# Kernel tuning notes

Measured on AMD Instinct MI355X. Metric: run time of the kernel, lower is better.

## Reference

```python
import jax, jax.numpy as jnp
import numpy as np

N_NODES = 50000
N_EDGES = 800000
N_HOPS = 4  # layers + 1
NFEAT, NHID, NOUT = 256, 128, 64


def setup_inputs() -> dict:
    key = jax.random.key(0)
    ks = jax.random.split(key, 8)
    x = jax.random.normal(ks[0], (N_NODES, NFEAT), dtype=jnp.float32)
    W = jax.random.normal(ks[1], (N_HOPS, NFEAT, NHID), dtype=jnp.float32) * 0.05
    b = jax.random.normal(ks[2], (N_HOPS, NHID), dtype=jnp.float32) * 0.05
    W_out = jax.random.normal(ks[3], (NHID * N_HOPS, NOUT), dtype=jnp.float32) * 0.05
    b_out = jax.random.normal(ks[4], (NOUT,), dtype=jnp.float32) * 0.05
    edge_rows = jax.random.randint(ks[5], (N_HOPS, N_EDGES), 0, N_NODES, dtype=jnp.int32)
    edge_cols = jax.random.randint(ks[6], (N_HOPS, N_EDGES), 0, N_NODES, dtype=jnp.int32)
    edge_vals = jax.random.uniform(ks[7], (N_HOPS, N_EDGES), dtype=jnp.float32)
    return {"x": x, "W": W, "b": b, "W_out": W_out, "b_out": b_out,
            "edge_rows": edge_rows, "edge_cols": edge_cols, "edge_vals": edge_vals}


def reference(x, W, b, W_out, b_out, edge_rows, edge_cols, edge_vals):
    # per-hop linear: [N, nfeat] x [K, nfeat, nhid] -> [K, N, nhid]
    h = jnp.einsum('nf,kfh->knh', x, W) + b[:, None, :]

    def spmm(rows, cols, vals, feat):
        # COO spmm: out[r] += vals[e] * feat[cols[e]]
        return jax.ops.segment_sum(vals[:, None] * feat[cols], rows,
                                   num_segments=N_NODES)

    agg = jax.vmap(spmm)(edge_rows, edge_cols, edge_vals, h)  # [K, N, nhid]
    # concat across hops along feature dim (matches torch.cat order)
    concat = jnp.transpose(agg, (1, 0, 2)).reshape(x.shape[0], -1)  # [N, K*nhid]
    z = jax.nn.elu(concat)
    return z @ W_out + b_out  # [N, nout]
```

## Files before the change

### kernel.cpp

```cpp
#include <hip/hip_runtime.h>
#include <hip/hip_bf16.h>
#include <math.h>

#define NNODES 50000
#define NPAD   50176
#define NEDGES 800000
#define NHOPS  4
#define NF     256
#define NH     128
#define NO     64
#define NB     196
#define EPB    4096

#define CONVX_BLOCKS 12500
#define CONVW_BLOCKS 512
#define HIST1_BLOCKS (NB * NHOPS)
#define WOT_BLOCKS   128
#define LIN_PER_HOP  391
#define LIN_BLOCKS   1568
#define ASTR 40
#define CPAD 132

typedef __attribute__((ext_vector_type(8))) short bfrag_t;
typedef __attribute__((ext_vector_type(4))) float facc_t;

static __device__ __forceinline__ unsigned short f2bf(float f) {
  unsigned int u = __float_as_uint(f);
  unsigned int r = (u + 0x7fffu + ((u >> 16) & 1u)) >> 16;
  return (unsigned short)r;
}
static __device__ __forceinline__ float bf2f_lo(unsigned int u) {
  return __uint_as_float(u << 16);
}
static __device__ __forceinline__ float bf2f_hi(unsigned int u) {
  return __uint_as_float(u & 0xffff0000u);
}

__global__ __launch_bounds__(256) void phaseA_kernel(
    const float* __restrict__ x, unsigned short* __restrict__ xb,
    const float* __restrict__ W, unsigned short* __restrict__ Wt,
    const int* __restrict__ erows, int* __restrict__ bucketCur,
    const float* __restrict__ Wout, unsigned short* __restrict__ wot) {
  const int bx = blockIdx.x;
  const int t  = threadIdx.x;
  if (bx < CONVX_BLOCKS) {
    const size_t i = ((size_t)bx * 256 + t) * 4;
    float4 v = *(const float4*)&x[i];
    ushort4 o;
    o.x = f2bf(v.x); o.y = f2bf(v.y); o.z = f2bf(v.z); o.w = f2bf(v.w);
    *(ushort4*)&xb[i] = o;
  } else if (bx < CONVX_BLOCKS + CONVW_BLOCKS) {
    const int i = (bx - CONVX_BLOCKS) * 256 + t;
    const int k = i / (NH * NF);
    const int rem = i - k * NH * NF;
    const int n = rem / NF;
    const int f = rem - n * NF;
    Wt[i] = f2bf(W[(size_t)k * NF * NH + (size_t)f * NH + n]);
  } else if (bx < CONVX_BLOCKS + CONVW_BLOCKS + HIST1_BLOCKS) {
    const int id  = bx - (CONVX_BLOCKS + CONVW_BLOCKS);
    const int hop = id / NB;
    const int bb  = (id - hop * NB) * EPB;
    __shared__ int bh[NB];
    for (int i = t; i < NB; i += 256) bh[i] = 0;
    __syncthreads();
    const size_t g0 = (size_t)hop * NEDGES;
#pragma unroll
    for (int k = 0; k < 4; ++k) {
      const int e0 = bb + t * 4 + k * 1024;
      if (e0 + 3 < NEDGES) {
        const int4 rr = *(const int4*)&erows[g0 + e0];
        atomicAdd(&bh[rr.x >> 8], 1);
        atomicAdd(&bh[rr.y >> 8], 1);
        atomicAdd(&bh[rr.z >> 8], 1);
        atomicAdd(&bh[rr.w >> 8], 1);
      } else {
        for (int j = 0; j < 4; ++j)
          if (e0 + j < NEDGES) atomicAdd(&bh[erows[g0 + e0 + j] >> 8], 1);
      }
    }
    __syncthreads();
    for (int i = t; i < NB; i += 256)
      if (bh[i]) atomicAdd(&bucketCur[hop * NB + i], bh[i]);
  } else {
    const int i = (bx - (CONVX_BLOCKS + CONVW_BLOCKS + HIST1_BLOCKS)) * 256 + t;
    const int o = i & 63;
    const int f = i >> 6;
    wot[(size_t)o * 512 + f] = f2bf(Wout[(size_t)f * NO + o]);
  }
}

__global__ __launch_bounds__(256) void scanB_kernel(
    int* __restrict__ bucketCur, int* __restrict__ bucketBase) {
  const int hop = blockIdx.x;
  const int t   = threadIdx.x;
  __shared__ int tot[NB];
  for (int i = t; i < NB; i += 256) tot[i] = bucketCur[hop * NB + i];
  __syncthreads();
  if (t == 0) {
    int run = 0;
    for (int i = 0; i < NB; ++i) { const int c = tot[i]; tot[i] = run; run += c; }
  }
  __syncthreads();
  for (int i = t; i < NB; i += 256) {
    bucketCur[hop * NB + i]        = tot[i];
    bucketBase[hop * (NB + 1) + i] = tot[i];
  }
  if (t == 0) bucketBase[hop * (NB + 1) + NB] = NEDGES;
}

__global__ __launch_bounds__(256) void linear_kernel(
    const unsigned short* __restrict__ xb, const unsigned short* __restrict__ Wt,
    const float* __restrict__ b, unsigned short* __restrict__ slots) {
  const int lb  = blockIdx.x;
  const int g   = lb >> 5;
  const int rr_ = lb & 31;
  const int hop = rr_ >> 3;
  const int xx  = rr_ & 7;
  const int mb  = g * 8 + xx;
  if (mb >= LIN_PER_HOP) return;
  const unsigned short* Wk = Wt + (size_t)hop * NH * NF;
  const float* bk = b + hop * NH;
  unsigned short* hb = slots + (size_t)(hop + 1) * NNODES * NH;

  const int t    = threadIdx.x;
  const int lane = t & 63;
  const int wave = t >> 6;
  const int wm   = (wave >> 1) * 64;
  const int wn   = (wave & 1) * 64;
  const int m0   = mb * 128;
  const int l15  = lane & 15;
  const int quad = lane >> 4;

  __shared__ unsigned short smem[10240];
  unsigned short* as_ = smem;
  unsigned short* cs  = smem;

  facc_t acc[4][4];
#pragma unroll
  for (int i = 0; i < 4; ++i)
#pragma unroll
    for (int j = 0; j < 4; ++j) {
      facc_t z = {0.f, 0.f, 0.f, 0.f};
      acc[i][j] = z;
    }

#pragma unroll
  for (int k0 = 0; k0 < NF; k0 += 32) {
    __syncthreads();
#pragma unroll
    for (int it = 0; it < 2; ++it) {
      const int row = it * 64 + (t >> 2);
      const int ch  = t & 3;
      const uint4 v = *(const uint4*)&xb[(size_t)(m0 + row) * NF + k0 + ch * 8];
      *(uint4*)&as_[row * ASTR + ch * 8] = v;
    }
    __syncthreads();

    bfrag_t a[4], bb[4];
#pragma unroll
    for (int mi = 0; mi < 4; ++mi)
      a[mi] = *(const bfrag_t*)&as_[(wm + mi * 16 + l15) * ASTR + quad * 8];
#pragma unroll
    for (int ni = 0; ni < 4; ++ni) {
      const int n = wn + ni * 16 + l15;
      bb[ni] = *(const bfrag_t*)&Wk[(size_t)n * NF + k0 + quad * 8];
    }
#pragma unroll
    for (int mi = 0; mi < 4; ++mi)
#pragma unroll
      for (int ni = 0; ni < 4; ++ni)
        acc[mi][ni] = __builtin_amdgcn_mfma_f32_16x16x32_bf16(
            a[mi], bb[ni], acc[mi][ni], 0, 0, 0);
  }

#pragma unroll
  for (int half = 0; half < 2; ++half) {
    __syncthreads();
    if ((wave >> 1) == half) {
#pragma unroll
      for (int ni = 0; ni < 4; ++ni) {
        const int nl = wn + ni * 16 + l15;
        const float bias = bk[nl];
#pragma unroll
        for (int mi = 0; mi < 4; ++mi) {
#pragma unroll
          for (int r = 0; r < 4; ++r) {
            const int ml = mi * 16 + quad * 4 + r;
            cs[ml * CPAD + nl] = f2bf(acc[mi][ni][r] + bias);
          }
        }
      }
    }
    __syncthreads();
    const int chunk = t & 15;
    const int rowb  = t >> 4;
#pragma unroll
    for (int it = 0; it < 4; ++it) {
      const int row = it * 16 + rowb;
      const int m   = m0 + half * 64 + row;
      const uint4 v = *(const uint4*)&cs[row * CPAD + chunk * 8];
      if (m < NNODES) *(uint4*)&hb[(size_t)m * NH + chunk * 8] = v;
    }
  }
}

__global__ __launch_bounds__(256) void bin_kernel(
    const int* __restrict__ erows, const int* __restrict__ ecols,
    const float* __restrict__ evals, int* __restrict__ bucketCur,
    unsigned long long* __restrict__ staging) {
  const int hop = blockIdx.y;
  const int t   = threadIdx.x;
  const int bb  = blockIdx.x * EPB;
  __shared__ int lhist[NB];
  __shared__ int gbase[NB];
  for (int i = t; i < NB; i += 256) lhist[i] = 0;
  __syncthreads();

  unsigned long long pk[16];
  int bkt[16], rnk[16];
  const size_t g0 = (size_t)hop * NEDGES;
#pragma unroll
  for (int k = 0; k < 4; ++k) {
    const int e0 = bb + t * 4 + k * 1024;
    if (e0 + 3 < NEDGES) {
      const int4   rr = *(const int4*)&erows[g0 + e0];
      const int4   cc = *(const int4*)&ecols[g0 + e0];
      const float4 vv = *(const float4*)&evals[g0 + e0];
      const int r4[4] = {rr.x, rr.y, rr.z, rr.w};
      const int c4[4] = {cc.x, cc.y, cc.z, cc.w};
      const float v4[4] = {vv.x, vv.y, vv.z, vv.w};
#pragma unroll
      for (int j = 0; j < 4; ++j) {
        const int b = r4[j] >> 8;
        bkt[k * 4 + j] = b;
        rnk[k * 4 + j] = atomicAdd(&lhist[b], 1);
        pk[k * 4 + j] =
            ((unsigned long long)__float_as_uint(v4[j]) << 32) |
            ((unsigned)(r4[j] & 255) << 16) | (unsigned)c4[j];
      }
    } else {
#pragma unroll
      for (int j = 0; j < 4; ++j) {
        const int e = e0 + j;
        if (e < NEDGES) {
          const int r = erows[g0 + e];
          const int b = r >> 8;
          bkt[k * 4 + j] = b;
          rnk[k * 4 + j] = atomicAdd(&lhist[b], 1);
          pk[k * 4 + j] =
              ((unsigned long long)__float_as_uint(evals[g0 + e]) << 32) |
              ((unsigned)(r & 255) << 16) | (unsigned)ecols[g0 + e];
        } else {
          bkt[k * 4 + j] = -1;
        }
      }
    }
  }
  __syncthreads();
  for (int i = t; i < NB; i += 256) {
    const int c = lhist[i];
    gbase[i] = c ? atomicAdd(&bucketCur[hop * NB + i], c) : 0;
  }
  __syncthreads();
  unsigned long long* dst = staging + (size_t)hop * NEDGES;
#pragma unroll
  for (int q = 0; q < 16; ++q)
    if (bkt[q] >= 0) dst[gbase[bkt[q]] + rnk[q]] = pk[q];
}

__global__ __launch_bounds__(256) void countscan_kernel(
    const int* __restrict__ bucketBase,
    const unsigned long long* __restrict__ staging, int* __restrict__ counts) {
  const int hop = blockIdx.y;
  const int b   = blockIdx.x;
  const int t   = threadIdx.x;
  const int s = bucketBase[hop * (NB + 1) + b];
  const int e = bucketBase[hop * (NB + 1) + b + 1];
  __shared__ int h[256];
  h[t] = 0;
  __syncthreads();
  const unsigned long long* src = staging + (size_t)hop * NEDGES;
  for (int i = s + t; i < e; i += 256) {
    const int rl = ((unsigned)src[i] >> 16) & 255;
    atomicAdd(&h[rl], 1);
  }
  __syncthreads();
  const int r0 = b * 256;
  if (r0 + t < NNODES) counts[hop * NNODES + r0 + t] = h[t];
}

__global__ __launch_bounds__(1024) void scan_kernel(
    const int* __restrict__ counts, int* __restrict__ offs) {
  const int hop  = blockIdx.x;
  const int t    = threadIdx.x;
  const int lane = t & 63;
  const int wid  = t >> 6;
  __shared__ int wsum[16];
  __shared__ int carry_s;
  if (t == 0) carry_s = 0;
  __syncthreads();
  const int CH  = 8192;
  const int nch = (NNODES + CH - 1) / CH;
  for (int ch = 0; ch < nch; ++ch) {
    const int i0 = ch * CH + t * 8;
    int v[8];
    if (i0 + 7 < NNODES) {
      int4 a = *(const int4*)&counts[hop * NNODES + i0];
      int4 b = *(const int4*)&counts[hop * NNODES + i0 + 4];
      v[0]=a.x; v[1]=a.y; v[2]=a.z; v[3]=a.w;
      v[4]=b.x; v[5]=b.y; v[6]=b.z; v[7]=b.w;
    } else {
#pragma unroll
      for (int j = 0; j < 8; ++j)
        v[j] = (i0 + j < NNODES) ? counts[hop * NNODES + i0 + j] : 0;
    }
    int l[8];
    int run = 0;
#pragma unroll
    for (int j = 0; j < 8; ++j) { run += v[j]; l[j] = run; }
    int s = run;
#pragma unroll
    for (int d = 1; d < 64; d <<= 1) {
      int n = __shfl_up(s, d, 64);
      if (lane >= d) s += n;
    }
    if (lane == 63) wsum[wid] = s;
    __syncthreads();
    if (t < 16) {
      int ws = wsum[t];
#pragma unroll
      for (int d = 1; d < 16; d <<= 1) {
        int n = __shfl_up(ws, d, 16);
        if (t >= d) ws += n;
      }
      wsum[t] = ws;
    }
    __syncthreads();
    const int base = carry_s + (wid ? wsum[wid - 1] : 0) + (s - run);
    if (i0 + 7 < NNODES) {
      int4 o0 = make_int4(base, base + l[0], base + l[1], base + l[2]);
      int4 o1 = make_int4(base + l[3], base + l[4], base + l[5], base + l[6]);
      *(int4*)&offs[hop * (NNODES + 1) + i0]     = o0;
      *(int4*)&offs[hop * (NNODES + 1) + i0 + 4] = o1;
    } else {
#pragma unroll
      for (int j = 0; j < 8; ++j) {
        if (i0 + j < NNODES) {
          const int excl = base + (l[j] - v[j]);
          offs[hop * (NNODES + 1) + i0 + j] = excl;
        }
      }
    }
    __syncthreads();
    if (t == 0) carry_s += wsum[15];
    __syncthreads();
  }
  if (t == 0) offs[hop * (NNODES + 1) + NNODES] = carry_s;
}

__global__ __launch_bounds__(256) void place_kernel(
    const int* __restrict__ offs, const unsigned long long* __restrict__ staging,
    unsigned long long* __restrict__ ecsr) {
  const int hop = blockIdx.y;
  const int bk  = blockIdx.x;
  const int t   = threadIdx.x;
  const int r0  = bk * 256;
  const int nr  = (NNODES - r0 < 256) ? (NNODES - r0) : 256;
  const int* o = offs + (size_t)hop * (NNODES + 1);
  __shared__ int cur[257];
  for (int i = t; i <= nr; i += 256) cur[i] = o[r0 + i];
  __syncthreads();
  const int s = cur[0];
  const int e = cur[nr];
  __syncthreads();
  const unsigned long long* src = staging + (size_t)hop * NEDGES;
  unsigned long long* dst       = ecsr + (size_t)hop * NEDGES;
  for (int i = s + t; i < e; i += 256) {
    const unsigned long long v = src[i];
    const unsigned lo = (unsigned)v;
    const int rl = (lo >> 16) & 255;
    const int d = atomicAdd(&cur[rl], 1);
    dst[d] = (v & 0xFFFFFFFF00000000ull) | (unsigned long long)(lo & 0xFFFFu);
  }
}

__global__ __launch_bounds__(256) void gather_kernel(
    const int* __restrict__ offs, const int2* __restrict__ ecsr,
    const unsigned short* __restrict__ hb, unsigned short* __restrict__ aggb) {
  const int t    = threadIdx.x;
  const int lane = t & 63;
  const int wid  = t >> 6;
  const int r = blockIdx.x * 4 + wid;
  const int g  = lane >> 4;
  const int sl = lane & 15;
  const int s = offs[r];
  const int e = offs[r + 1];

  float acc[8];
#pragma unroll
  for (int j = 0; j < 8; ++j) acc[j] = 0.f;

  for (int p = s; p < e; p += 16) {
    int2 ed[4];
#pragma unroll
    for (int q = 0; q < 4; ++q) {
      const int idx = p + q * 4 + g;
      ed[q] = (idx < e) ? ecsr[idx] : make_int2(0, 0);
    }
    uint4 hv[4];
#pragma unroll
    for (int q = 0; q < 4; ++q)
      hv[q] = *(const uint4*)&hb[(size_t)ed[q].x * NH + sl * 8];
#pragma unroll
    for (int q = 0; q < 4; ++q) {
      const float v = __int_as_float(ed[q].y);
      acc[0] += v * bf2f_lo(hv[q].x);
      acc[1] += v * bf2f_hi(hv[q].x);
      acc[2] += v * bf2f_lo(hv[q].y);
      acc[3] += v * bf2f_hi(hv[q].y);
      acc[4] += v * bf2f_lo(hv[q].z);
      acc[5] += v * bf2f_hi(hv[q].z);
      acc[6] += v * bf2f_lo(hv[q].w);
      acc[7] += v * bf2f_hi(hv[q].w);
    }
  }

#pragma unroll
  for (int j = 0; j < 8; ++j) {
    acc[j] += __shfl_xor(acc[j], 16, 64);
    acc[j] += __shfl_xor(acc[j], 32, 64);
  }

  if (g == 0) {
    uint4 o;
    o.x = (unsigned)f2bf(acc[0]) | ((unsigned)f2bf(acc[1]) << 16);
    o.y = (unsigned)f2bf(acc[2]) | ((unsigned)f2bf(acc[3]) << 16);
    o.z = (unsigned)f2bf(acc[4]) | ((unsigned)f2bf(acc[5]) << 16);
    o.w = (unsigned)f2bf(acc[6]) | ((unsigned)f2bf(acc[7]) << 16);
    *(uint4*)&aggb[(size_t)r * NH + sl * 8] = o;
  }
}

__global__ __launch_bounds__(256) void out2_kernel(
    const unsigned short* __restrict__ aggb,
    const unsigned short* __restrict__ wot,
    const float* __restrict__ bout, float* __restrict__ out) {
  const int t    = threadIdx.x;
  const int lane = t & 63;
  const int wave = t >> 6;
  const int l15  = lane & 15;
  const int quad = lane >> 4;
  const int m0   = blockIdx.x * 64 + wave * 16;

  facc_t acc[4];
#pragma unroll
  for (int ni = 0; ni < 4; ++ni) { facc_t z = {0.f,0.f,0.f,0.f}; acc[ni] = z; }

  const int mrow  = m0 + l15;
  const int mload = mrow < NNODES ? mrow : NNODES - 1;

#pragma unroll
  for (int ks = 0; ks < 16; ++ks) {
    const int f0  = ks * 32 + quad * 8;
    const int hop = f0 >> 7;
    const int j0  = f0 & 127;
    uint4 ua = *(const uint4*)&aggb[((size_t)hop * NNODES + mload) * NH + j0];
    const unsigned uu[4] = {ua.x, ua.y, ua.z, ua.w};
    unsigned pr[4];
#pragma unroll
    for (int q = 0; q < 4; ++q) {
      float lo = bf2f_lo(uu[q]);
      float hi = bf2f_hi(uu[q]);
      lo = lo > 0.f ? lo : (expf(lo) - 1.f);
      hi = hi > 0.f ? hi : (expf(hi) - 1.f);
      pr[q] = (unsigned)f2bf(lo) | ((unsigned)f2bf(hi) << 16);
    }
    uint4 ra; ra.x = pr[0]; ra.y = pr[1]; ra.z = pr[2]; ra.w = pr[3];
    bfrag_t af = *(bfrag_t*)&ra;
    bfrag_t bf[4];
#pragma unroll
    for (int ni = 0; ni < 4; ++ni) {
      const int n = ni * 16 + l15;
      bf[ni] = *(const bfrag_t*)&wot[(size_t)n * 512 + f0];
    }
#pragma unroll
    for (int ni = 0; ni < 4; ++ni)
      acc[ni] = __builtin_amdgcn_mfma_f32_16x16x32_bf16(af, bf[ni], acc[ni], 0, 0, 0);
  }

#pragma unroll
  for (int ni = 0; ni < 4; ++ni) {
    const int o = ni * 16 + l15;
    const float bo = bout[o];
#pragma unroll
    for (int r = 0; r < 4; ++r) {
      const int m = m0 + quad * 4 + r;
      if (m < NNODES) out[(size_t)m * NO + o] = acc[ni][r] + bo;
    }
  }
}

extern "C" void kernel_launch(void* const* d_in, const int* in_sizes, int n_in,
                              void* d_out, int out_size, void* d_ws, size_t ws_size,
                              hipStream_t stream) {
  const float* x     = (const float*)d_in[0];
  const float* W     = (const float*)d_in[1];
  const float* b     = (const float*)d_in[2];
  const float* W_out = (const float*)d_in[3];
  const float* b_out = (const float*)d_in[4];
  const int*   erows = (const int*)d_in[5];
  const int*   ecols = (const int*)d_in[6];
  const float* evals = (const float*)d_in[7];
  float* out = (float*)d_out;

  unsigned short* slots = (unsigned short*)d_ws;
  unsigned short* xb = slots + (size_t)(NHOPS + 1) * NNODES * NH;
  unsigned short* Wt = xb + (size_t)NPAD * NF;
  unsigned long long* ecsr = (unsigned long long*)(Wt + (size_t)NHOPS * NH * NF);
  int* counts     = (int*)(ecsr + (size_t)NHOPS * NEDGES);
  int* offs       = counts + NHOPS * NNODES;
  int* bucketCur  = offs + NHOPS * (NNODES + 1);
  int* bucketBase = bucketCur + NHOPS * NB;
  unsigned short* wot = (unsigned short*)(bucketBase + NHOPS * (NB + 1));
  unsigned long long* staging = (unsigned long long*)xb;

  hipMemsetAsync(bucketCur, 0, (size_t)NHOPS * NB * sizeof(int), stream);

  phaseA_kernel<<<CONVX_BLOCKS + CONVW_BLOCKS + HIST1_BLOCKS + WOT_BLOCKS,
                  256, 0, stream>>>(x, xb, W, Wt, erows, bucketCur, W_out, wot);
  scanB_kernel<<<NHOPS, 256, 0, stream>>>(bucketCur, bucketBase);
  linear_kernel<<<LIN_BLOCKS, 256, 0, stream>>>(xb, Wt, b, slots);
  bin_kernel<<<dim3(NB, NHOPS), 256, 0, stream>>>(
      erows, ecols, evals, bucketCur, staging);
  countscan_kernel<<<dim3(NB, NHOPS), 256, 0, stream>>>(
      bucketBase, staging, counts);
  scan_kernel<<<NHOPS, 1024, 0, stream>>>(counts, offs);
  place_kernel<<<dim3(NB, NHOPS), 256, 0, stream>>>(offs, staging, ecsr);

  for (int k = 0; k < NHOPS; ++k) {
    gather_kernel<<<NNODES / 4, 256, 0, stream>>>(
        offs + (size_t)k * (NNODES + 1), (const int2*)(ecsr + (size_t)k * NEDGES),
        slots + (size_t)(k + 1) * NNODES * NH,
        slots + (size_t)k * NNODES * NH);
  }

  out2_kernel<<<782, 256, 0, stream>>>(slots, wot, b_out, out);
}
```

Measured before the change: 437.4 us.

## Batch hop gathers into paired launches and load GEMM A-fragments directly

Gathers for two hops now run in one 2D-grid launch. Outputs for hops 1 and 3 are redirected into the dead xb buffer so they do not overwrite inputs still being read, and out2 takes four separate aggregation pointers. The linear kernel drops LDS staging of the x tile and loads MFMA A-fragments straight from global memory, removing barriers but with less coalesced loads.

New measurement: 435.1 us. Within noise of the previous version (-0.5%).

```diff
diff --git a/kernel.cpp b/kernel.cpp
--- a/kernel.cpp
+++ b/kernel.cpp
@@ -18,7 +18,6 @@
 #define WOT_BLOCKS   128
 #define LIN_PER_HOP  391
 #define LIN_BLOCKS   1568
-#define ASTR 40
 #define CPAD 132
 
 typedef __attribute__((ext_vector_type(8))) short bfrag_t;
@@ -131,9 +130,7 @@
   const int l15  = lane & 15;
   const int quad = lane >> 4;
 
-  __shared__ unsigned short smem[10240];
-  unsigned short* as_ = smem;
-  unsigned short* cs  = smem;
+  __shared__ unsigned short cs[64 * CPAD];
 
   facc_t acc[4][4];
 #pragma unroll
@@ -146,20 +143,12 @@
 
 #pragma unroll
   for (int k0 = 0; k0 < NF; k0 += 32) {
-    __syncthreads();
-#pragma unroll
-    for (int it = 0; it < 2; ++it) {
-      const int row = it * 64 + (t >> 2);
-      const int ch  = t & 3;
-      const uint4 v = *(const uint4*)&xb[(size_t)(m0 + row) * NF + k0 + ch * 8];
-      *(uint4*)&as_[row * ASTR + ch * 8] = v;
-    }
-    __syncthreads();
-
     bfrag_t a[4], bb[4];
 #pragma unroll
-    for (int mi = 0; mi < 4; ++mi)
-      a[mi] = *(const bfrag_t*)&as_[(wm + mi * 16 + l15) * ASTR + quad * 8];
+    for (int mi = 0; mi < 4; ++mi) {
+      const int m = m0 + wm + mi * 16 + l15;
+      a[mi] = *(const bfrag_t*)&xb[(size_t)m * NF + k0 + quad * 8];
+    }
 #pragma unroll
     for (int ni = 0; ni < 4; ++ni) {
       const int n = wn + ni * 16 + l15;
@@ -384,17 +373,26 @@
   }
 }
 
-__global__ __launch_bounds__(256) void gather_kernel(
+__global__ __launch_bounds__(256) void gather2_kernel(
     const int* __restrict__ offs, const int2* __restrict__ ecsr,
-    const unsigned short* __restrict__ hb, unsigned short* __restrict__ aggb) {
+    const unsigned short* __restrict__ slots,
+    unsigned short* __restrict__ aggA, unsigned short* __restrict__ aggB,
+    int hop0) {
+  const int y    = blockIdx.y;
+  const int hop  = hop0 + y;
+  const int* off = offs + (size_t)hop * (NNODES + 1);
+  const int2* ec = ecsr + (size_t)hop * NEDGES;
+  const unsigned short* hb = slots + (size_t)(hop + 1) * NNODES * NH;
+  unsigned short* aggb = y ? aggB : aggA;
+
   const int t    = threadIdx.x;
   const int lane = t & 63;
   const int wid  = t >> 6;
   const int r = blockIdx.x * 4 + wid;
   const int g  = lane >> 4;
   const int sl = lane & 15;
-  const int s = offs[r];
-  const int e = offs[r + 1];
+  const int s = off[r];
+  const int e = off[r + 1];
 
   float acc[8];
 #pragma unroll
@@ -405,7 +403,7 @@
 #pragma unroll
     for (int q = 0; q < 4; ++q) {
       const int idx = p + q * 4 + g;
-      ed[q] = (idx < e) ? ecsr[idx] : make_int2(0, 0);
+      ed[q] = (idx < e) ? ec[idx] : make_int2(0, 0);
     }
     uint4 hv[4];
 #pragma unroll
@@ -442,7 +440,8 @@
 }
 
 __global__ __launch_bounds__(256) void out2_kernel(
-    const unsigned short* __restrict__ aggb,
+    const unsigned short* __restrict__ agg0, const unsigned short* __restrict__ agg1,
+    const unsigned short* __restrict__ agg2, const unsigned short* __restrict__ agg3,
     const unsigned short* __restrict__ wot,
     const float* __restrict__ bout, float* __restrict__ out) {
   const int t    = threadIdx.x;
@@ -464,7 +463,9 @@
     const int f0  = ks * 32 + quad * 8;
     const int hop = f0 >> 7;
     const int j0  = f0 & 127;
-    uint4 ua = *(const uint4*)&aggb[((size_t)hop * NNODES + mload) * NH + j0];
+    const unsigned short* ab =
+        (hop == 0) ? agg0 : (hop == 1) ? agg1 : (hop == 2) ? agg2 : agg3;
+    uint4 ua = *(const uint4*)&ab[(size_t)mload * NH + j0];
     const unsigned uu[4] = {ua.x, ua.y, ua.z, ua.w};
     unsigned pr[4];
 #pragma unroll
@@ -523,6 +524,8 @@
   int* bucketBase = bucketCur + NHOPS * NB;
   unsigned short* wot = (unsigned short*)(bucketBase + NHOPS * (NB + 1));
   unsigned long long* staging = (unsigned long long*)xb;
+  unsigned short* agg1buf = xb;
+  unsigned short* agg3buf = xb + (size_t)NNODES * NH;
 
   hipMemsetAsync(bucketCur, 0, (size_t)NHOPS * NB * sizeof(int), stream);
 
@@ -537,12 +540,12 @@
   scan_kernel<<<NHOPS, 1024, 0, stream>>>(counts, offs);
   place_kernel<<<dim3(NB, NHOPS), 256, 0, stream>>>(offs, staging, ecsr);
 
-  for (int k = 0; k < NHOPS; ++k) {
-    gather_kernel<<<NNODES / 4, 256, 0, stream>>>(
-        offs + (size_t)k * (NNODES + 1), (const int2*)(ecsr + (size_t)k * NEDGES),
-        slots + (size_t)(k + 1) * NNODES * NH,
-        slots + (size_t)k * NNODES * NH);
-  }
-
-  out2_kernel<<<782, 256, 0, stream>>>(slots, wot, b_out, out);
-}
+  gather2_kernel<<<dim3(NNODES / 4, 2), 256, 0, stream>>>(
+      offs, (const int2*)ecsr, slots, slots , agg1buf, 0);
+  gather2_kernel<<<dim3(NNODES / 4, 2), 256, 0, stream>>>(
+      offs, (const int2*)ecsr, slots, slots + (size_t)2 * NNODES * NH, agg3buf, 2);
+
+  out2_kernel<<<782, 256, 0, stream>>>(
+      slots, agg1buf, slots + (size_t)2 * NNODES * NH, agg3buf,
+      wot, b_out, out);
+}
```
